# Kernel optimization log

Hardware: AMD Instinct MI355X
Metric: run time of the kernel (lower is better)

## Reference

```python
import jax, jax.numpy as jnp
import numpy as np

B = 512
V = 6890   # SMPL vertices
NJ = 24    # joints (global)
NB = 10    # shape betas
NP = 207   # pose blendshape features = 23*9
NJO = 19   # cocoplus output joints
PARENTS = np.array([0,0,0,0,1,2,3,4,5,6,7,8,9,9,9,12,13,14,16,17,18,19,20,21], dtype=np.int32)


def setup_inputs() -> dict:
    key = jax.random.key(0)
    ks = jax.random.split(key, 7)
    inputs = jax.random.normal(ks[0], (B, 82), jnp.float32) * 0.2  # [pose(72) | shape(10)]
    v_template = jax.random.normal(ks[1], (V, 3), jnp.float32)
    shapes = jax.random.normal(ks[2], (NB, V * 3), jnp.float32) * 0.01
    posedirs = jax.random.normal(ks[3], (NP, V * 3), jnp.float32) * 0.01
    jr = jax.random.uniform(ks[4], (V, NJ), jnp.float32)
    smpl_regressor = jr / jnp.sum(jr, axis=0, keepdims=True)          # columns sum to 1 over vertices
    w = jax.random.uniform(ks[5], (V, NJ), jnp.float32) ** 4
    lbs_weights = w / jnp.sum(w, axis=1, keepdims=True)               # rows sum to 1 over joints
    cr = jax.random.uniform(ks[6], (V, NJO), jnp.float32)
    joint_regressor = cr / jnp.sum(cr, axis=0, keepdims=True)
    parents = jnp.asarray(PARENTS)
    return {"inputs": inputs, "v_template": v_template, "shapes": shapes,
            "posedirs": posedirs, "smpl_regressor": smpl_regressor,
            "lbs_weights": lbs_weights, "joint_regressor": joint_regressor,
            "parents": parents}


def _rodrigues(pose):  # [B,72] -> [B,24,3,3]
    r = pose.reshape(-1, 3)
    angle = jnp.linalg.norm(r + 1e-8, axis=1, keepdims=True)  # [N,1]
    n = r / angle
    c = jnp.cos(angle)[:, :, None]   # [N,1,1]
    s = jnp.sin(angle)[:, :, None]
    outer = n[:, :, None] * n[:, None, :]
    z = jnp.zeros_like(n[:, 0])
    K = jnp.stack([z, -n[:, 2], n[:, 1],
                   n[:, 2], z, -n[:, 0],
                   -n[:, 1], n[:, 0], z], axis=1).reshape(-1, 3, 3)
    R = c * jnp.eye(3, dtype=pose.dtype) + (1.0 - c) * outer + s * K
    return R.reshape(-1, NJ, 3, 3)


def _make_A(R, t):  # R [B,3,3], t [B,3] -> [B,4,4]
    top = jnp.concatenate([R, t[:, :, None]], axis=2)
    bottom = jnp.broadcast_to(jnp.array([0., 0., 0., 1.], dtype=R.dtype), (R.shape[0], 1, 4))
    return jnp.concatenate([top, bottom], axis=1)


def _global_rigid(rotations, joints, parents_np):
    # sequential kinematic-chain composition over the fixed 24-joint tree
    res = [_make_A(rotations[:, 0], joints[:, 0])]
    for i in range(1, NJ):
        p = int(parents_np[i])
        t = joints[:, i] - joints[:, p]
        res.append(jnp.matmul(res[p], _make_A(rotations[:, i], t)))
    A_world = jnp.stack(res, axis=1)                 # [B,24,4,4]
    new_J = A_world[:, :, :3, 3]
    Jw0 = jnp.concatenate([joints, jnp.zeros(joints.shape[:2] + (1,), joints.dtype)], axis=2)[..., None]
    init_bone = jnp.matmul(A_world, Jw0)[..., 0]     # [B,24,4]
    pad = jnp.zeros_like(A_world).at[:, :, :, 3].set(init_bone)
    return new_J, A_world - pad


def reference(inputs, v_template, shapes, posedirs, smpl_regressor, lbs_weights, joint_regressor, parents):
    b = inputs.shape[0]
    pose = inputs[:, :72]
    beta = inputs[:, -10:]
    v_shaped = jnp.matmul(beta, shapes).reshape(b, V, 3) + v_template
    v_joints = jnp.einsum('bvc,vj->bjc', v_shaped, smpl_regressor)        # [B,24,3]
    rot = _rodrigues(pose)                                                # [B,24,3,3]
    pose_feature = (rot[:, 1:] - jnp.eye(3, dtype=rot.dtype)).reshape(b, -1)  # [B,207]
    v_posed = jnp.matmul(pose_feature, posedirs).reshape(b, V, 3) + v_shaped
    joint_transformed, A = _global_rigid(rot, v_joints, np.asarray(parents))
    T = jnp.einsum('vj,bjk->bvk', lbs_weights, A.reshape(b, NJ, 16)).reshape(b, V, 4, 4)
    v_homo = jnp.concatenate([v_posed, jnp.ones((b, V, 1), v_posed.dtype)], axis=2)
    vertices = jnp.einsum('bvij,bvj->bvi', T, v_homo)[:, :, :3]
    joints = jnp.einsum('bvc,vj->bjc', vertices, joint_regressor)         # [B,19,3]
    return vertices, joints, rot
```

## Files before the change

### kernel.cpp

```cpp
#include <hip/hip_runtime.h>

#define B_   512
#define V_   6890
#define V3_  20670
#define NJ_  24
#define NB_  10
#define NP_  207
#define NJO_ 19

typedef __attribute__((ext_vector_type(8))) short short8;
typedef __attribute__((ext_vector_type(8))) __bf16 bf16x8;
typedef __attribute__((ext_vector_type(4))) float f32x4;


#define SRB_   192
#define SRCH_  862
#define RODB_  48
#define TRB_   26

__global__ void __launch_bounds__(256) k_pre(const float* __restrict__ in,
                                             const float* __restrict__ shapes,
                                             const float* __restrict__ vt,
                                             const float* __restrict__ sreg,
                                             const float* __restrict__ jreg,
                                             float* __restrict__ srtr,
                                             float* __restrict__ out_rot,
                                             float* __restrict__ pf_t,
                                             float* __restrict__ jreg_t,
                                             float* __restrict__ jout) {
  int blk = blockIdx.x;
  int tid = threadIdx.x;
  if (blk < SRB_) {
    int j  = blk >> 3;
    int ch = blk & 7;
    int vend = (ch + 1) * SRCH_; if (vend > V_) vend = V_;
    float acc[33];
#pragma unroll
    for (int a = 0; a < 33; a++) acc[a] = 0.f;
    for (int v = ch * SRCH_ + tid; v < vend; v += 256) {
      float w = sreg[v * NJ_ + j];
#pragma unroll
      for (int k = 0; k < NB_; k++) {
        const float* sp = shapes + k * V3_ + 3 * v;
#pragma unroll
        for (int c = 0; c < 3; c++) acc[k * 3 + c] += w * sp[c];
      }
#pragma unroll
      for (int c = 0; c < 3; c++) acc[30 + c] += w * vt[3 * v + c];
    }
    __shared__ float red[4][33];
    int wave = tid >> 6, lane = tid & 63;
#pragma unroll
    for (int a = 0; a < 33; a++) {
      float x = acc[a];
#pragma unroll
      for (int m = 1; m < 64; m <<= 1) x += __shfl_xor(x, m, 64);
      if (lane == 0) red[wave][a] = x;
    }
    __syncthreads();
    if (tid < 33) {
      float s = red[0][tid] + red[1][tid] + red[2][tid] + red[3][tid];
      if (tid < 30) atomicAdd(&srtr[((tid / 3) * NJ_ + j) * 3 + (tid % 3)], s);
      else          atomicAdd(&srtr[720 + j * 3 + (tid - 30)], s);
    }
  } else if (blk < SRB_ + RODB_) {
    int idx = (blk - SRB_) * 256 + tid;
    int b = idx & (B_ - 1);
    int j = idx >> 9;
    const float* r = in + b * 82 + j * 3;
    float r0 = r[0], r1 = r[1], r2 = r[2];
    float ax = r0 + 1e-8f, ay = r1 + 1e-8f, az = r2 + 1e-8f;
    float angle = sqrtf(ax * ax + ay * ay + az * az);
    float inv = 1.0f / angle;
    float n0 = r0 * inv, n1 = r1 * inv, n2 = r2 * inv;
    float c = cosf(angle), s = sinf(angle);
    float ic = 1.0f - c;
    float R[9];
    R[0] = c + ic * n0 * n0;      R[1] = ic * n0 * n1 - s * n2;  R[2] = ic * n0 * n2 + s * n1;
    R[3] = ic * n1 * n0 + s * n2; R[4] = c + ic * n1 * n1;       R[5] = ic * n1 * n2 - s * n0;
    R[6] = ic * n2 * n0 - s * n1; R[7] = ic * n2 * n1 + s * n0;  R[8] = c + ic * n2 * n2;
    float* ro = out_rot + b * 216 + j * 9;
#pragma unroll
    for (int q = 0; q < 9; q++) ro[q] = R[q];
    if (j > 0) {
#pragma unroll
      for (int q = 0; q < 9; q++)
        pf_t[(size_t)((j - 1) * 9 + q) * B_ + b] = R[q] - ((q % 4 == 0) ? 1.0f : 0.0f);
    }
  } else {
    int idx = (blk - SRB_ - RODB_) * 256 + tid;
    for (int q = idx; q < B_ * NJO_ * 3; q += TRB_ * 256) jout[q] = 0.f;
    for (int e = idx; e < V_ * NJO_; e += TRB_ * 256) {
      int jo = e / V_;
      int v  = e - jo * V_;
      jreg_t[e] = jreg[v * NJO_ + jo];
    }
  }
}

__global__ void __launch_bounds__(192) k_chain(const float* __restrict__ in,
                                               const float* __restrict__ rot,
                                               const float* __restrict__ srtr,
                                               const int* __restrict__ parents,
                                               float* __restrict__ Abuf) {
  (void)parents;
  constexpr int P[NJ_] = {0, 0, 0, 0, 1, 2, 3, 4, 5, 6, 7, 8, 9, 9, 9, 12, 13, 14,
                          16, 17, 18, 19, 20, 21};
  int tid = threadIdx.x;
  int bl = tid & 63;
  int r  = tid >> 6;
  int b  = blockIdx.x * 64 + bl;
  float beta[NB_];
#pragma unroll
  for (int k = 0; k < NB_; k++) beta[k] = in[b * 82 + 72 + k];
  float J[NJ_][3];
#pragma unroll
  for (int j = 0; j < NJ_; j++) {
#pragma unroll
    for (int c = 0; c < 3; c++) {
      float s = srtr[720 + j * 3 + c];
#pragma unroll
      for (int k = 0; k < NB_; k++) s += beta[k] * srtr[(k * NJ_ + j) * 3 + c];
      J[j][c] = s;
    }
  }
  const float* Rb = rot + b * 216;
  float A[NJ_][4];
#pragma unroll
  for (int c = 0; c < 3; c++) A[0][c] = Rb[r * 3 + c];
  A[0][3] = J[0][r];
#pragma unroll
  for (int j = 1; j < NJ_; j++) {
    const int p = P[j];
    float t0 = J[j][0] - J[p][0];
    float t1 = J[j][1] - J[p][1];
    float t2 = J[j][2] - J[p][2];
    float Rj[9];
#pragma unroll
    for (int q = 0; q < 9; q++) Rj[q] = Rb[j * 9 + q];
    float p0 = A[p][0], p1 = A[p][1], p2 = A[p][2], p3 = A[p][3];
#pragma unroll
    for (int c = 0; c < 3; c++)
      A[j][c] = p0 * Rj[c] + p1 * Rj[3 + c] + p2 * Rj[6 + c];
    A[j][3] = p0 * t0 + p1 * t1 + p2 * t2 + p3;
  }
  float* Ab = Abuf + (size_t)b * 288 + r * 4;
#pragma unroll
  for (int j = 0; j < NJ_; j++) {
    float4 o;
    o.x = A[j][0]; o.y = A[j][1]; o.z = A[j][2];
    o.w = A[j][3] - (A[j][0] * J[j][0] + A[j][1] * J[j][1] + A[j][2] * J[j][2]);
    *reinterpret_cast<float4*>(Ab + j * 12) = o;
  }
}

#define PB_   8
#define BT_   32
#define GX_   108
#define GY_   16
#define NWG_  (GX_ * GY_)
#define NKT_  7
#define UST_  5
#define BUFS_ (192 * UST_ * 8)
#define VPST_ 196

__device__ __forceinline__ unsigned short f2bf(float x) {
  unsigned int u = __builtin_bit_cast(unsigned int, x);
  u += 0x7fffu + ((u >> 16) & 1u);
  return (unsigned short)(u >> 16);
}

__device__ __forceinline__ f32x4 mfma_bf16(short8 a, short8 b, f32x4 c) {
  return __builtin_amdgcn_mfma_f32_16x16x32_bf16(
      __builtin_bit_cast(bf16x8, a), __builtin_bit_cast(bf16x8, b), c, 0, 0, 0);
}

__global__ void __launch_bounds__(256) k_main(const float* __restrict__ in,
                                              const float* __restrict__ shapes,
                                              const float* __restrict__ vt,
                                              const float* __restrict__ posedirs,
                                              const float* __restrict__ lbs,
                                              const float* __restrict__ pf_t,
                                              const float* __restrict__ Abuf,
                                              float* __restrict__ verts) {
  __shared__ float smem[2 * BUFS_ / 2];
  __shared__ float lbs_l[64 * 25];
  unsigned short* pds = reinterpret_cast<unsigned short*>(smem);

  int tid = threadIdx.x;
  int raw  = blockIdx.y * GX_ + blockIdx.x;
  int virt = (raw & 7) * (NWG_ / 8) + (raw >> 3);
  int vblk = virt >> 4;
  int bblk = virt & (GY_ - 1);
  int v0 = vblk * 64;
  int b0 = bblk * BT_;
  int nv = V_ - v0; if (nv > 64) nv = 64;
  for (int i = tid; i < nv * NJ_; i += 256)
    lbs_l[(i / NJ_) * 25 + (i % NJ_)] = lbs[(size_t)v0 * NJ_ + i];

  int lane = tid & 63;
  int g = tid >> 6;
  int v = v0 + lane;
  int vc = v < V_ ? v : V_ - 1;
  int ebase  = 3 * v0;
  int ebaseC = ebase; if (ebaseC > V3_ - 192) ebaseC = V3_ - 192;
  int lsh = ebase - ebaseC;

  int mt = g & 1;
  int nbase = (g >> 1) * 6;
  int bA = b0 + mt * 16 + (lane & 15);
  int kgrp = (lane >> 4) * 8;
  short8 afrag[NKT_];
#pragma unroll
  for (int kt = 0; kt < NKT_; kt++) {
    short8 a;
#pragma unroll
    for (int j = 0; j < 8; j++) {
      int rg = kt * 32 + kgrp + j;
      float fv = (rg < NP_) ? pf_t[(size_t)rg * B_ + bA] : 0.f;
      a[j] = (short)f2bf(fv);
    }
    afrag[kt] = a;
  }

  int sk  = tid >> 5;
  int se  = tid & 31;
  int ktlS = sk >> 1;
  int kloS = (sk & 1) * 4;

  {
    float2 sv[4][3];
#pragma unroll
    for (int kk = 0; kk < 4; kk++) {
      int rg = sk * 4 + kk; if (rg > NP_ - 1) rg = NP_ - 1;
      const float2* s2 = reinterpret_cast<const float2*>(posedirs + (size_t)rg * V3_ + ebaseC + se * 6);
#pragma unroll
      for (int q = 0; q < 3; q++) sv[kk][q] = s2[q];
    }
    unsigned short* pw = pds;
#pragma unroll
    for (int q = 0; q < 6; q++) {
      float v0f = (q & 1) ? sv[0][q >> 1].y : sv[0][q >> 1].x;
      float v1f = (q & 1) ? sv[1][q >> 1].y : sv[1][q >> 1].x;
      float v2f = (q & 1) ? sv[2][q >> 1].y : sv[2][q >> 1].x;
      float v3f = (q & 1) ? sv[3][q >> 1].y : sv[3][q >> 1].x;
      uint2 w;
      w.x = (unsigned)f2bf(v0f) | ((unsigned)f2bf(v1f) << 16);
      w.y = (unsigned)f2bf(v2f) | ((unsigned)f2bf(v3f) << 16);
      *reinterpret_cast<uint2*>(pw + ((se * 6 + q) * UST_ + ktlS) * 8 + kloS) = w;
    }
  }
  __syncthreads();

  f32x4 acc[6];
#pragma unroll
  for (int n = 0; n < 6; n++) acc[n] = {0.f, 0.f, 0.f, 0.f};
  int ktlL = lane >> 4;
  int eLb  = (lane & 15);

  for (int c = 0; c < NKT_; c++) {
    float2 sv[4][3];
    const bool more = (c + 1 < NKT_);
    if (more) {
#pragma unroll
      for (int kk = 0; kk < 4; kk++) {
        int rg = (c + 1) * 32 + sk * 4 + kk; if (rg > NP_ - 1) rg = NP_ - 1;
        const float2* s2 = reinterpret_cast<const float2*>(posedirs + (size_t)rg * V3_ + ebaseC + se * 6);
#pragma unroll
        for (int q = 0; q < 3; q++) sv[kk][q] = s2[q];
      }
    }
    const unsigned short* pr = pds + (c & 1) * BUFS_;
#pragma unroll
    for (int n = 0; n < 6; n++) {
      int eL = (nbase + n) * 16 + eLb;
      short8 bfrg = *reinterpret_cast<const short8*>(pr + (eL * UST_ + ktlL) * 8);
      acc[n] = mfma_bf16(afrag[c], bfrg, acc[n]);
    }
    if (more) {
      unsigned short* pw = pds + ((c + 1) & 1) * BUFS_;
#pragma unroll
      for (int q = 0; q < 6; q++) {
        float v0f = (q & 1) ? sv[0][q >> 1].y : sv[0][q >> 1].x;
        float v1f = (q & 1) ? sv[1][q >> 1].y : sv[1][q >> 1].x;
        float v2f = (q & 1) ? sv[2][q >> 1].y : sv[2][q >> 1].x;
        float v3f = (q & 1) ? sv[3][q >> 1].y : sv[3][q >> 1].x;
        uint2 w;
        w.x = (unsigned)f2bf(v0f) | ((unsigned)f2bf(v1f) << 16);
        w.y = (unsigned)f2bf(v2f) | ((unsigned)f2bf(v3f) << 16);
        *reinterpret_cast<uint2*>(pw + ((se * 6 + q) * UST_ + ktlS) * 8 + kloS) = w;
      }
    }
    __syncthreads();
  }

#pragma unroll
  for (int n = 0; n < 6; n++) {
    int ecol = (nbase + n) * 16 + eLb;
#pragma unroll
    for (int reg = 0; reg < 4; reg++) {
      int brow = mt * 16 + (lane >> 4) * 4 + reg;
      smem[brow * VPST_ + ecol] = acc[n][reg];
    }
  }
  __syncthreads();

  int bb0 = __builtin_amdgcn_readfirstlane(b0 + g * PB_);
  int li = 3 * lane + lsh; if (v >= V_) li = 0;

  float acc2[PB_][3];
  {
    float t0 = vt[3 * vc + 0], t1 = vt[3 * vc + 1], t2 = vt[3 * vc + 2];
#pragma unroll
    for (int i = 0; i < PB_; i++) {
      int bl = g * PB_ + i;
      acc2[i][0] = t0 + smem[bl * VPST_ + li + 0];
      acc2[i][1] = t1 + smem[bl * VPST_ + li + 1];
      acc2[i][2] = t2 + smem[bl * VPST_ + li + 2];
    }
  }
#pragma unroll
  for (int k = 0; k < NB_; k++) {
    const float* sp = shapes + k * V3_ + 3 * vc;
    float s0 = sp[0], s1 = sp[1], s2 = sp[2];
#pragma unroll
    for (int i = 0; i < PB_; i++) {
      float bv = in[(size_t)(bb0 + i) * 82 + 72 + k];
      acc2[i][0] += bv * s0; acc2[i][1] += bv * s1; acc2[i][2] += bv * s2;
    }
  }
  float o[PB_][3];
#pragma unroll
  for (int i = 0; i < PB_; i++) { o[i][0] = 0.f; o[i][1] = 0.f; o[i][2] = 0.f; }
  for (int j = 0; j < NJ_; j++) {
    float w = lbs_l[lane * 25 + j];
#pragma unroll
    for (int i = 0; i < PB_; i++) {
      const float4* M4 = reinterpret_cast<const float4*>(Abuf + (size_t)(bb0 + i) * 288 + j * 12);
      float4 m0 = M4[0], m1 = M4[1], m2 = M4[2];
      float x = acc2[i][0], y = acc2[i][1], z = acc2[i][2];
      o[i][0] += w * (m0.x * x + m0.y * y + m0.z * z + m0.w);
      o[i][1] += w * (m1.x * x + m1.y * y + m1.z * z + m1.w);
      o[i][2] += w * (m2.x * x + m2.y * y + m2.z * z + m2.w);
    }
  }
  if (v < V_) {
#pragma unroll
    for (int i = 0; i < PB_; i++) {
      float* op = verts + (size_t)(bb0 + i) * (V_ * 3) + 3 * v;
      op[0] = o[i][0]; op[1] = o[i][1]; op[2] = o[i][2];
    }
  }
}

#define JCH_ 1728
__global__ void __launch_bounds__(256) k_joints(const float* __restrict__ verts,
                                                const float* __restrict__ jreg_t,
                                                float* __restrict__ jout) {
  int b = blockIdx.x;
  int ch = blockIdx.y;
  int tid = threadIdx.x;
  int vend = (ch + 1) * JCH_; if (vend > V_) vend = V_;
  float acc[NJO_ * 3];
#pragma unroll
  for (int a = 0; a < NJO_ * 3; a++) acc[a] = 0.f;
  const float* vb = verts + (size_t)b * V_ * 3;
  for (int v = ch * JCH_ + tid; v < vend; v += 256) {
    float x = vb[3 * v + 0], y = vb[3 * v + 1], z = vb[3 * v + 2];
#pragma unroll
    for (int jo = 0; jo < NJO_; jo++) {
      float w = jreg_t[jo * V_ + v];
      acc[jo * 3 + 0] += w * x; acc[jo * 3 + 1] += w * y; acc[jo * 3 + 2] += w * z;
    }
  }
  __shared__ float red[4][NJO_ * 3];
  int wave = tid >> 6, lane = tid & 63;
#pragma unroll
  for (int a = 0; a < NJO_ * 3; a++) {
    float x = acc[a];
#pragma unroll
    for (int m = 1; m < 64; m <<= 1) x += __shfl_xor(x, m, 64);
    if (lane == 0) red[wave][a] = x;
  }
  __syncthreads();
  if (tid < NJO_ * 3) {
    float s = red[0][tid] + red[1][tid] + red[2][tid] + red[3][tid];
    atomicAdd(&jout[b * (NJO_ * 3) + tid], s);
  }
}

extern "C" void kernel_launch(void* const* d_in, const int* in_sizes, int n_in,
                              void* d_out, int out_size, void* d_ws, size_t ws_size,
                              hipStream_t stream) {
  const float* inputs   = (const float*)d_in[0];
  const float* v_templ  = (const float*)d_in[1];
  const float* shapes   = (const float*)d_in[2];
  const float* posedirs = (const float*)d_in[3];
  const float* sreg     = (const float*)d_in[4];
  const float* lbs      = (const float*)d_in[5];
  const float* jreg     = (const float*)d_in[6];
  const int*   parents  = (const int*)d_in[7];

  float* out   = (float*)d_out;
  float* verts = out;
  float* jout  = out + 10583040;
  float* rot   = out + 10612224;

  float* ws     = (float*)d_ws;
  float* pf_t   = ws;
  float* Abuf   = ws + 105984;
  float* srtr   = ws + 105984 + 147456;
  float* jreg_t = srtr + 792;

  hipMemsetAsync(srtr, 0, 792 * sizeof(float), stream);

  k_pre  <<<SRB_ + RODB_ + TRB_, 256, 0, stream>>>(inputs, shapes, v_templ, sreg, jreg,
                                                   srtr, rot, pf_t, jreg_t, jout);
  k_chain<<<8, 192, 0, stream>>>(inputs, rot, srtr, parents, Abuf);
  dim3 gmain(GX_, GY_);
  k_main <<<gmain, 256, 0, stream>>>(inputs, shapes, v_templ, posedirs, lbs, pf_t, Abuf, verts);
  dim3 gj(B_, 4);
  k_joints<<<gj, 256, 0, stream>>>(verts, jreg_t, jout);
}
```

Before: 241.7 us.

## Replace atomic regressor reduction with per-chunk partials and widen posedirs LDS staging

k_pre now writes each chunk's shape-regressor partial sums to its own slice of an 8-way buffer instead of atomically accumulating. k_chain sums those slices into shared memory first, which lets the host drop the hipMemsetAsync and its extra stream operation. In k_main, each thread now stages 8 k-rows by 3 elements of posedirs and packs them into one 16-byte LDS store per element, instead of 4 k-rows with 8-byte stores. The global loads become scalar rather than float2, which may change load efficiency.

```diff
diff --git a/kernel.cpp b/kernel.cpp
--- a/kernel.cpp
+++ b/kernel.cpp
@@ -23,7 +23,7 @@
                                              const float* __restrict__ vt,
                                              const float* __restrict__ sreg,
                                              const float* __restrict__ jreg,
-                                             float* __restrict__ srtr,
+                                             float* __restrict__ srtr8,
                                              float* __restrict__ out_rot,
                                              float* __restrict__ pf_t,
                                              float* __restrict__ jreg_t,
@@ -60,8 +60,9 @@
     __syncthreads();
     if (tid < 33) {
       float s = red[0][tid] + red[1][tid] + red[2][tid] + red[3][tid];
-      if (tid < 30) atomicAdd(&srtr[((tid / 3) * NJ_ + j) * 3 + (tid % 3)], s);
-      else          atomicAdd(&srtr[720 + j * 3 + (tid - 30)], s);
+      float* dst = srtr8 + ch * 792;
+      if (tid < 30) dst[((tid / 3) * NJ_ + j) * 3 + (tid % 3)] = s;
+      else          dst[720 + j * 3 + (tid - 30)] = s;
     }
   } else if (blk < SRB_ + RODB_) {
     int idx = (blk - SRB_) * 256 + tid;
@@ -100,13 +101,21 @@
 
 __global__ void __launch_bounds__(192) k_chain(const float* __restrict__ in,
                                                const float* __restrict__ rot,
-                                               const float* __restrict__ srtr,
+                                               const float* __restrict__ srtr8,
                                                const int* __restrict__ parents,
                                                float* __restrict__ Abuf) {
   (void)parents;
   constexpr int P[NJ_] = {0, 0, 0, 0, 1, 2, 3, 4, 5, 6, 7, 8, 9, 9, 9, 12, 13, 14,
                           16, 17, 18, 19, 20, 21};
+  __shared__ float srl[792];
   int tid = threadIdx.x;
+  for (int i = tid; i < 792; i += 192) {
+    float s = 0.f;
+#pragma unroll
+    for (int ch = 0; ch < 8; ch++) s += srtr8[ch * 792 + i];
+    srl[i] = s;
+  }
+  __syncthreads();
   int bl = tid & 63;
   int r  = tid >> 6;
   int b  = blockIdx.x * 64 + bl;
@@ -118,9 +127,9 @@
   for (int j = 0; j < NJ_; j++) {
 #pragma unroll
     for (int c = 0; c < 3; c++) {
-      float s = srtr[720 + j * 3 + c];
-#pragma unroll
-      for (int k = 0; k < NB_; k++) s += beta[k] * srtr[(k * NJ_ + j) * 3 + c];
+      float s = srl[720 + j * 3 + c];
+#pragma unroll
+      for (int k = 0; k < NB_; k++) s += beta[k] * srl[(k * NJ_ + j) * 3 + c];
       J[j][c] = s;
     }
   }
@@ -164,10 +173,10 @@
 #define BUFS_ (192 * UST_ * 8)
 #define VPST_ 196
 
-__device__ __forceinline__ unsigned short f2bf(float x) {
+__device__ __forceinline__ unsigned f2bf(float x) {
   unsigned int u = __builtin_bit_cast(unsigned int, x);
   u += 0x7fffu + ((u >> 16) & 1u);
-  return (unsigned short)(u >> 16);
+  return u >> 16;
 }
 
 __device__ __forceinline__ f32x4 mfma_bf16(short8 a, short8 b, f32x4 c) {
@@ -183,7 +192,7 @@
                                               const float* __restrict__ pf_t,
                                               const float* __restrict__ Abuf,
                                               float* __restrict__ verts) {
-  __shared__ float smem[2 * BUFS_ / 2];
+  __shared__ float smem[BUFS_];
   __shared__ float lbs_l[64 * 25];
   unsigned short* pds = reinterpret_cast<unsigned short*>(smem);
 
@@ -223,31 +232,26 @@
     afrag[kt] = a;
   }
 
-  int sk  = tid >> 5;
-  int se  = tid & 31;
-  int ktlS = sk >> 1;
-  int kloS = (sk & 1) * 4;
+  const int kg = g;
+  const int e0 = lane * 3;
 
   {
-    float2 sv[4][3];
-#pragma unroll
-    for (int kk = 0; kk < 4; kk++) {
-      int rg = sk * 4 + kk; if (rg > NP_ - 1) rg = NP_ - 1;
-      const float2* s2 = reinterpret_cast<const float2*>(posedirs + (size_t)rg * V3_ + ebaseC + se * 6);
-#pragma unroll
-      for (int q = 0; q < 3; q++) sv[kk][q] = s2[q];
+    float sv[8][3];
+#pragma unroll
+    for (int kk = 0; kk < 8; kk++) {
+      int rg = kg * 8 + kk; if (rg > NP_ - 1) rg = NP_ - 1;
+      const float* src = posedirs + (size_t)rg * V3_ + ebaseC + e0;
+      sv[kk][0] = src[0]; sv[kk][1] = src[1]; sv[kk][2] = src[2];
     }
     unsigned short* pw = pds;
 #pragma unroll
-    for (int q = 0; q < 6; q++) {
-      float v0f = (q & 1) ? sv[0][q >> 1].y : sv[0][q >> 1].x;
-      float v1f = (q & 1) ? sv[1][q >> 1].y : sv[1][q >> 1].x;
-      float v2f = (q & 1) ? sv[2][q >> 1].y : sv[2][q >> 1].x;
-      float v3f = (q & 1) ? sv[3][q >> 1].y : sv[3][q >> 1].x;
-      uint2 w;
-      w.x = (unsigned)f2bf(v0f) | ((unsigned)f2bf(v1f) << 16);
-      w.y = (unsigned)f2bf(v2f) | ((unsigned)f2bf(v3f) << 16);
-      *reinterpret_cast<uint2*>(pw + ((se * 6 + q) * UST_ + ktlS) * 8 + kloS) = w;
+    for (int j = 0; j < 3; j++) {
+      uint4 w;
+      w.x = f2bf(sv[0][j]) | (f2bf(sv[1][j]) << 16);
+      w.y = f2bf(sv[2][j]) | (f2bf(sv[3][j]) << 16);
+      w.z = f2bf(sv[4][j]) | (f2bf(sv[5][j]) << 16);
+      w.w = f2bf(sv[6][j]) | (f2bf(sv[7][j]) << 16);
+      *reinterpret_cast<uint4*>(pw + ((e0 + j) * UST_ + kg) * 8) = w;
     }
   }
   __syncthreads();
@@ -259,15 +263,14 @@
   int eLb  = (lane & 15);
 
   for (int c = 0; c < NKT_; c++) {
-    float2 sv[4][3];
+    float sv[8][3];
     const bool more = (c + 1 < NKT_);
     if (more) {
 #pragma unroll
-      for (int kk = 0; kk < 4; kk++) {
-        int rg = (c + 1) * 32 + sk * 4 + kk; if (rg > NP_ - 1) rg = NP_ - 1;
-        const float2* s2 = reinterpret_cast<const float2*>(posedirs + (size_t)rg * V3_ + ebaseC + se * 6);
-#pragma unroll
-        for (int q = 0; q < 3; q++) sv[kk][q] = s2[q];
+      for (int kk = 0; kk < 8; kk++) {
+        int rg = (c + 1) * 32 + kg * 8 + kk; if (rg > NP_ - 1) rg = NP_ - 1;
+        const float* src = posedirs + (size_t)rg * V3_ + ebaseC + e0;
+        sv[kk][0] = src[0]; sv[kk][1] = src[1]; sv[kk][2] = src[2];
       }
     }
     const unsigned short* pr = pds + (c & 1) * BUFS_;
@@ -280,15 +283,13 @@
     if (more) {
       unsigned short* pw = pds + ((c + 1) & 1) * BUFS_;
 #pragma unroll
-      for (int q = 0; q < 6; q++) {
-        float v0f = (q & 1) ? sv[0][q >> 1].y : sv[0][q >> 1].x;
-        float v1f = (q & 1) ? sv[1][q >> 1].y : sv[1][q >> 1].x;
-        float v2f = (q & 1) ? sv[2][q >> 1].y : sv[2][q >> 1].x;
-        float v3f = (q & 1) ? sv[3][q >> 1].y : sv[3][q >> 1].x;
-        uint2 w;
-        w.x = (unsigned)f2bf(v0f) | ((unsigned)f2bf(v1f) << 16);
-        w.y = (unsigned)f2bf(v2f) | ((unsigned)f2bf(v3f) << 16);
-        *reinterpret_cast<uint2*>(pw + ((se * 6 + q) * UST_ + ktlS) * 8 + kloS) = w;
+      for (int j = 0; j < 3; j++) {
+        uint4 w;
+        w.x = f2bf(sv[0][j]) | (f2bf(sv[1][j]) << 16);
+        w.y = f2bf(sv[2][j]) | (f2bf(sv[3][j]) << 16);
+        w.z = f2bf(sv[4][j]) | (f2bf(sv[5][j]) << 16);
+        w.w = f2bf(sv[6][j]) | (f2bf(sv[7][j]) << 16);
+        *reinterpret_cast<uint4*>(pw + ((e0 + j) * UST_ + kg) * 8) = w;
       }
     }
     __syncthreads();
@@ -409,14 +410,12 @@
   float* ws     = (float*)d_ws;
   float* pf_t   = ws;
   float* Abuf   = ws + 105984;
-  float* srtr   = ws + 105984 + 147456;
-  float* jreg_t = srtr + 792;
-
-  hipMemsetAsync(srtr, 0, 792 * sizeof(float), stream);
+  float* srtr8  = ws + 105984 + 147456;
+  float* jreg_t = srtr8 + 6336;
 
   k_pre  <<<SRB_ + RODB_ + TRB_, 256, 0, stream>>>(inputs, shapes, v_templ, sreg, jreg,
-                                                   srtr, rot, pf_t, jreg_t, jout);
-  k_chain<<<8, 192, 0, stream>>>(inputs, rot, srtr, parents, Abuf);
+                                                   srtr8, rot, pf_t, jreg_t, jout);
+  k_chain<<<8, 192, 0, stream>>>(inputs, rot, srtr8, parents, Abuf);
   dim3 gmain(GX_, GY_);
   k_main <<<gmain, 256, 0, stream>>>(inputs, shapes, v_templ, posedirs, lbs, pf_t, Abuf, verts);
   dim3 gj(B_, 4);
```

Result: slower. 255.6 us (+5.7%).
